# Kernel optimization log

Measured on AMD Instinct MI355X. Metric: run time of the kernel, lower is better.

The kernel has to match this reference:

```python
import jax, jax.numpy as jnp
import numpy as np

B, DIM, H, W = 8, 384, 64, 64
HEADS = 8
D = DIM // HEADS          # 48
D2 = D // 2               # 24
DU = D // 3 * 2           # 32 (ratio=3)


def setup_inputs() -> dict:
    key = jax.random.key(0)
    ks = jax.random.split(key, 12)
    s = lambda k, shape, scale=0.05: jax.random.normal(k, shape, jnp.float32) * scale
    return {
        "x": jax.random.normal(ks[0], (B, DIM, H, W), jnp.float32),
        "temperature": jnp.ones((HEADS, 1, 1), jnp.float32),
        "w_qkv": s(ks[1], (3 * DIM, DIM)),          # 1x1 conv, no bias
        "w_dw": s(ks[2], (3 * DIM, 1, 3, 3)),       # depthwise 3x3, groups=3*dim
        "w_proj": s(ks[3], (DIM, HEADS)),           # project_out 1x1
        "w_attn_r": s(ks[4], (1, D)),
        "w_v_r": s(ks[5], (D2, D)),
        "w_up1": s(ks[6], (DU, D2)),
        "b_up1": jnp.zeros((DU,), jnp.float32),
        "ln_w": jnp.ones((DU, HEADS, 1), jnp.float32),
        "ln_b": jnp.zeros((DU, HEADS, 1), jnp.float32),
        "w_up2": s(ks[7], (D, DU)),
        "b_up2": jnp.zeros((D,), jnp.float32),
        "w_attn_l": s(ks[8], (D2, D)),
        "w_v_l": s(ks[9], (D2, D)),
    }


def _qkv_attn(x, temperature, w_qkv, w_dw):
    # shared: qkv 1x1 conv -> depthwise 3x3 -> split, normalize, elementwise attn+softmax
    b, c, h, w = x.shape
    qkv = jnp.einsum('bchw,oc->bohw', x, w_qkv)
    qkv = jax.lax.conv_general_dilated(
        qkv, w_dw, (1, 1), 'SAME', feature_group_count=3 * c,
        dimension_numbers=('NCHW', 'OIHW', 'NCHW'))
    q, k, v = jnp.split(qkv, 3, axis=1)
    rs = lambda t: t.reshape(b, HEADS, D, h * w)  # b (head d) h w -> b head d (hw)
    q, k, v = rs(q), rs(k), rs(v)
    qn = q / jnp.maximum(jnp.linalg.norm(q, axis=-1, keepdims=True), 1e-12)
    kn = k / jnp.maximum(jnp.linalg.norm(k, axis=-1, keepdims=True), 1e-12)
    attn = jax.nn.softmax(qn * kn * temperature, axis=-1)  # [b, head, d, s]
    return attn, v


def _forward(x, temperature, w_qkv, w_dw, w_proj, w_attn_r, w_v_r,
             w_up1, b_up1, ln_w, ln_b, w_up2, b_up2, w_attn_l, w_v_l):
    b, c, h, w = x.shape
    attn, v = _qkv_attn(x, temperature, w_qkv, w_dw)

    # ---- spatial_pool (channel gating) ----
    input_x = jnp.einsum('bhds,od->bhos', v, w_v_r)                 # conv_v_right: [b,head,d2,s]
    cm = jax.nn.softmax(jnp.einsum('bhds,d->bhs', attn, w_attn_r[0]), axis=-1)  # conv_attn_right + softmax
    ctx = jnp.einsum('bhs,bhjs->bhj', cm, input_x)                  # [b,head,d2]
    ctx = ctx.transpose(0, 2, 1)[..., None]                         # [b, d2, head, 1]
    u = jnp.einsum('bchl,oc->bohl', ctx, w_up1) + b_up1[None, :, None, None]  # [b, DU, head, 1]
    mu = u.mean(axis=(1, 2, 3), keepdims=True)
    var = u.var(axis=(1, 2, 3), keepdims=True)
    u = (u - mu) / jnp.sqrt(var + 1e-5) * ln_w[None] + ln_b[None]   # LayerNorm([DU, 8, 1])
    u = jax.nn.relu(u)
    u = jnp.einsum('bchl,oc->bohl', u, w_up2) + b_up2[None, :, None, None]    # [b, D, head, 1]
    mask_ch = jax.nn.sigmoid(u).reshape(b, c, 1, 1)                 # view(b, head*D, 1, 1)
    out_channel = x * mask_ch

    # ---- channel_pool (spatial gating) ----
    g = jnp.einsum('bhds,od->bhos', attn, w_attn_l)                 # conv_attn_left: [b,head,d2,s]
    avg = jax.nn.softmax(g.mean(axis=-1), axis=-1)                  # avg-pool over s, softmax over d2
    theta = jnp.einsum('bhds,od->bhos', v, w_v_l)                   # conv_v_left: [b,head,d2,s]
    ctx2 = jnp.einsum('bhd,bhds->bhs', avg, theta)                  # matmul: [b,head,s]
    mask_sp = jax.nn.sigmoid(ctx2).reshape(b, HEADS, h, w)
    mask_sp = jnp.einsum('bchw,oc->bohw', mask_sp, w_proj)          # project_out
    out_spatial = x * mask_sp

    return out_spatial + out_channel


def reference(x, temperature, w_qkv, w_dw, w_proj, w_attn_r, w_v_r,
              w_up1, b_up1, ln_w, ln_b, w_up2, b_up2, w_attn_l, w_v_l):
    return _forward(x, temperature, w_qkv, w_dw, w_proj, w_attn_r, w_v_r,
                    w_up1, b_up1, ln_w, ln_b, w_up2, b_up2, w_attn_l, w_v_l)
```

## Files before the change

kernel.cpp:

```cpp
#include <hip/hip_runtime.h>
#include <math.h>


#define S4096 4096
#define C384  384
#define OC    1152

typedef unsigned short bfraw;
typedef unsigned int   u32;
typedef __attribute__((ext_vector_type(8))) short bf16x8;
typedef __attribute__((ext_vector_type(4))) float f32x4;

typedef __attribute__((address_space(3))) unsigned int lds_u32;
typedef const __attribute__((address_space(1))) unsigned int glb_u32;
__device__ __forceinline__ void gll16(const void* g, void* l) {
    __builtin_amdgcn_global_load_lds((glb_u32*)g, (lds_u32*)l, 16, 0, 0);
}

__device__ __forceinline__ bfraw f2bf(float f) {
    union { float f; u32 u; } c; c.f = f;
    u32 r = c.u + 0x7FFFu + ((c.u >> 16) & 1u);
    return (bfraw)(r >> 16);
}
__device__ __forceinline__ float bf2f(bfraw u) {
    union { u32 u; float f; } c; c.u = ((u32)u) << 16;
    return c.f;
}
__device__ __forceinline__ void unpack8(uint4 v, float* f) {
    f[0] = bf2f((bfraw)(v.x & 0xffff)); f[1] = bf2f((bfraw)(v.x >> 16));
    f[2] = bf2f((bfraw)(v.y & 0xffff)); f[3] = bf2f((bfraw)(v.y >> 16));
    f[4] = bf2f((bfraw)(v.z & 0xffff)); f[5] = bf2f((bfraw)(v.z >> 16));
    f[6] = bf2f((bfraw)(v.w & 0xffff)); f[7] = bf2f((bfraw)(v.w >> 16));
}
__device__ __forceinline__ uint4 pack8(const float* f) {
    union { bfraw us[8]; uint4 q; } p;
    #pragma unroll
    for (int i = 0; i < 8; i++) p.us[i] = f2bf(f[i]);
    return p.q;
}

__device__ __forceinline__ float blk_red(float v, float* s4, bool ismax) {
    #pragma unroll
    for (int off = 32; off; off >>= 1) {
        float o = __shfl_down(v, off, 64);
        v = ismax ? fmaxf(v, o) : (v + o);
    }
    __syncthreads();
    if ((threadIdx.x & 63) == 0) s4[threadIdx.x >> 6] = v;
    __syncthreads();
    return ismax ? fmaxf(fmaxf(s4[0], s4[1]), fmaxf(s4[2], s4[3]))
                 : ((s4[0] + s4[1]) + (s4[2] + s4[3]));
}

__global__ __launch_bounds__(256) void kA_prep(
    const float* __restrict__ w_qkv, bfraw* __restrict__ wF,
    const float* __restrict__ w_attn_l, const float* __restrict__ w_v_l,
    float* __restrict__ weff) {
    if (blockIdx.x == 216) {
        __shared__ float avg[24];
        const int tid = threadIdx.x;
        if (tid < 24) {
            float a = 0.f;
            for (int d = 0; d < 48; d++) a += w_attn_l[tid * 48 + d];
            avg[tid] = a * (1.f / 4096.f);
        }
        __syncthreads();
        if (tid == 0) {
            float M = -3.402823466e+38f;
            for (int o = 0; o < 24; o++) M = fmaxf(M, avg[o]);
            float S = 0.f;
            for (int o = 0; o < 24; o++) { avg[o] = __expf(avg[o] - M); S += avg[o]; }
            float inv = 1.f / S;
            for (int o = 0; o < 24; o++) avg[o] *= inv;
        }
        __syncthreads();
        if (tid < 48) {
            float a = 0.f;
            for (int o = 0; o < 24; o++) a += avg[o] * w_v_l[o * 48 + tid];
            weff[tid] = a;
        }
        return;
    }
    const int id = blockIdx.x * 256 + threadIdx.x;
    const int ob = id / 768, rem = id % 768;
    const int c = rem / 48, kb = rem % 48;
    const float* src = w_qkv + (size_t)(ob * 16 + c) * C384 + kb * 8;
    float f[8];
    *(float4*)f       = *(const float4*)src;
    *(float4*)(f + 4) = *(const float4*)(src + 4);
    *(uint4*)&wF[((size_t)(ob * 48 + kb) * 16 + c) * 8] = pack8(f);
}

__global__ __launch_bounds__(256) void kB_tr(
    const float* __restrict__ x, bfraw* __restrict__ xF, int b0) {
    const int cb = blockIdx.x, sb = blockIdx.y, bl = blockIdx.z;
    const int c0 = cb * 16, s0 = sb * 256;
    const int tid = threadIdx.x;
    __shared__ alignas(16) bfraw lt[16][264];
    {
        const int r = tid >> 4, seg = tid & 15;
        const float* src = x + ((size_t)(b0 + bl) * C384 + c0 + r) * S4096 + s0 + seg * 16;
        float f[16];
        #pragma unroll
        for (int i = 0; i < 4; i++) *(float4*)(f + i * 4) = *(const float4*)(src + i * 4);
        *(uint4*)&lt[r][seg * 16]     = pack8(f);
        *(uint4*)&lt[r][seg * 16 + 8] = pack8(f + 8);
    }
    __syncthreads();
    const int sbl = tid >> 4, c = tid & 15;
    bfraw* xFb = xF + (size_t)bl * S4096 * C384;
    #pragma unroll
    for (int kbl = 0; kbl < 2; kbl++) {
        union { bfraw us[8]; uint4 q; } p;
        #pragma unroll
        for (int j = 0; j < 8; j++) p.us[j] = lt[kbl * 8 + j][sbl * 16 + c];
        const size_t idx = (((size_t)((s0 >> 4) + sbl) * 48) + (c0 >> 3) + kbl) * 128 + c * 8;
        *(uint4*)&xFb[idx] = p.q;
    }
}

__global__ __launch_bounds__(256) void k1_gemm(
    const bfraw* __restrict__ wF, const bfraw* __restrict__ xF,
    bfraw* __restrict__ pre, int b0) {
    __shared__ alignas(16) bfraw smem[24576];
    const int tid = threadIdx.x;
    const int wave = tid >> 6, lane = tid & 63;
    const int sT = blockIdx.x, oT = blockIdx.y, bl = blockIdx.z;
    const bfraw* xFb = xF + (size_t)bl * S4096 * C384;

    const int c0_ = tid, c1_ = tid + 256;
    const int rb0 = c0_ >> 6, oc0 = (c0_ >> 4) & 3, rw0 = c0_ & 15;
    const int rb1 = c1_ >> 6, oc1 = (c1_ >> 4) & 3, rw1 = c1_ & 15;

    f32x4 acc[4][4];
    #pragma unroll
    for (int m = 0; m < 4; m++)
        #pragma unroll
        for (int n = 0; n < 4; n++) acc[m][n] = (f32x4){0, 0, 0, 0};

    const int wr = (wave >> 1) * 4;
    const int wc = (wave & 1) * 4;

    auto stage = [&](bfraw* dst, int kb0) {
        gll16(wF  + ((size_t)((oT * 8 + rb0) * 48 + kb0 + oc0) * 16 + rw0) * 8,
              dst + (size_t)c0_ * 8);
        gll16(wF  + ((size_t)((oT * 8 + rb1) * 48 + kb0 + oc1) * 16 + rw1) * 8,
              dst + (size_t)c1_ * 8);
        gll16(xFb + ((size_t)((sT * 8 + rb0) * 48 + kb0 + oc0) * 16 + rw0) * 8,
              dst + 4096 + (size_t)c0_ * 8);
        gll16(xFb + ((size_t)((sT * 8 + rb1) * 48 + kb0 + oc1) * 16 + rw1) * 8,
              dst + 4096 + (size_t)c1_ * 8);
    };

    stage(smem,        0);
    stage(smem + 8192, 4);

    #pragma unroll 3
    for (int ks = 0; ks < 12; ks++) {
        if (ks < 11) asm volatile("s_waitcnt vmcnt(4)" ::: "memory");
        else         asm volatile("s_waitcnt vmcnt(0)" ::: "memory");
        __builtin_amdgcn_s_barrier();
        const bfraw* cb = smem + (ks % 3) * 8192;
        bf16x8 af[4], bq[4];
        #pragma unroll
        for (int m = 0; m < 4; m++)
            af[m] = *(const bf16x8*)&cb[((wr + m) * 64 + lane) * 8];
        #pragma unroll
        for (int n = 0; n < 4; n++)
            bq[n] = *(const bf16x8*)&cb[4096 + ((wc + n) * 64 + lane) * 8];
        if (ks < 10) stage(smem + ((ks + 2) % 3) * 8192, (ks + 2) * 4);
        __builtin_amdgcn_s_setprio(1);
        #pragma unroll
        for (int m = 0; m < 4; m++)
            #pragma unroll
            for (int n = 0; n < 4; n++)
                acc[m][n] = __builtin_amdgcn_mfma_f32_16x16x32_bf16(af[m], bq[n], acc[m][n], 0, 0, 0);
        __builtin_amdgcn_s_setprio(0);
    }
    __syncthreads();

    const int er0 = (wave >> 1) * 64 + (lane >> 4) * 4;
    const int ec0 = (wave & 1) * 64 + (lane & 15);
    #pragma unroll
    for (int m = 0; m < 4; m++)
        #pragma unroll
        for (int n = 0; n < 4; n++)
            #pragma unroll
            for (int r = 0; r < 4; r++)
                smem[(er0 + m * 16 + r) * 136 + ec0 + n * 16] = f2bf(acc[m][n][r]);
    __syncthreads();
    const int row = tid >> 1, hh = tid & 1;
    bfraw* op = pre + (size_t)bl * OC * S4096
              + (size_t)(oT * 128 + row) * S4096 + sT * 128 + hh * 8;
    const bfraw* es = &smem[row * 136 + hh * 8];
    #pragma unroll
    for (int j = 0; j < 8; j++)
        *(uint4*)(op + j * 16) = *(const uint4*)(es + j * 16);
}

__device__ __forceinline__ void stencil8(const bfraw* plane, const float* w9,
                                         int ypad, int k7, int x0, float* acc) {
    #pragma unroll
    for (int j = 0; j < 8; j++) acc[j] = 0.f;
    #pragma unroll
    for (int dy = 0; dy < 3; dy++) {
        uint4 rv = *(const uint4*)&plane[(ypad + dy) * 64 + x0];
        float r[8]; unpack8(rv, r);
        float lft = __shfl_up(r[7], 1);
        float rgt = __shfl_down(r[0], 1);
        if (k7 == 0) lft = 0.f;
        if (k7 == 7) rgt = 0.f;
        const float w0 = w9[dy*3], w1 = w9[dy*3+1], w2 = w9[dy*3+2];
        acc[0] += w0*lft + w1*r[0] + w2*r[1];
        #pragma unroll
        for (int j = 1; j < 7; j++) acc[j] += w0*r[j-1] + w1*r[j] + w2*r[j+1];
        acc[7] += w0*r[6] + w1*r[7] + w2*rgt;
    }
}

__global__ __launch_bounds__(256) void k2f(
    const bfraw* __restrict__ pre, const float* __restrict__ w_dw,
    const float* __restrict__ temperature,
    bfraw* __restrict__ av, int b0) {
    const int idx = blockIdx.x;
    const int bl  = blockIdx.y;
    const int h   = idx / 48;
    const int tid = threadIdx.x;
    __shared__ alignas(16) bfraw pl[3][66 * 64];
    __shared__ float s4[4];

    const size_t pbase = (size_t)bl * OC * S4096;
    #pragma unroll
    for (int p = 0; p < 3; p++) {
        const bfraw* src = pre + pbase + (size_t)(idx + p * C384) * S4096;
        uint4 a = *(const uint4*)&src[tid * 16];
        uint4 b = *(const uint4*)&src[tid * 16 + 8];
        int y = tid >> 2, xq = (tid & 3) * 16;
        *(uint4*)&pl[p][(y + 1) * 64 + xq]     = a;
        *(uint4*)&pl[p][(y + 1) * 64 + xq + 8] = b;
    }
    if (tid < 64) {
        #pragma unroll
        for (int p = 0; p < 3; p++) { pl[p][tid] = 0; pl[p][65 * 64 + tid] = 0; }
    }
    float wq[9], wk[9], wv[9];
    #pragma unroll
    for (int i = 0; i < 9; i++) {
        wq[i] = w_dw[idx * 9 + i];
        wk[i] = w_dw[(idx + C384) * 9 + i];
        wv[i] = w_dw[(idx + 768) * 9 + i];
    }
    __syncthreads();

    const int sid0 = tid,        y0 = sid0 >> 3, k70 = sid0 & 7, x00 = k70 * 8;
    const int sid1 = tid + 256,  y1 = sid1 >> 3, k71 = sid1 & 7, x01 = k71 * 8;
    float qo[16], ko[16], vo[16];
    stencil8(pl[0], wq, y0, k70, x00, qo);
    stencil8(pl[0], wq, y1, k71, x01, qo + 8);
    stencil8(pl[1], wk, y0, k70, x00, ko);
    stencil8(pl[1], wk, y1, k71, x01, ko + 8);
    stencil8(pl[2], wv, y0, k70, x00, vo);
    stencil8(pl[2], wv, y1, k71, x01, vo + 8);

    float sq = 0.f, sk = 0.f;
    #pragma unroll
    for (int i = 0; i < 16; i++) { sq += qo[i] * qo[i]; sk += ko[i] * ko[i]; }
    float Sq = blk_red(sq, s4, false);
    float Sk = blk_red(sk, s4, false);
    float scale = temperature[h] /
        (fmaxf(sqrtf(Sq), 1e-12f) * fmaxf(sqrtf(Sk), 1e-12f));
    float lm = -3.402823466e+38f;
    #pragma unroll
    for (int i = 0; i < 16; i++) { qo[i] = qo[i] * ko[i] * scale; lm = fmaxf(lm, qo[i]); }
    float M = blk_red(lm, s4, true);
    float ls = 0.f;
    #pragma unroll
    for (int i = 0; i < 16; i++) { qo[i] = __expf(qo[i] - M); ls += qo[i]; }
    float Z = blk_red(ls, s4, false);
    float invZ = 1.f / Z;
    #pragma unroll
    for (int i = 0; i < 16; i++) qo[i] *= invZ;

    bfraw* adst = av + ((size_t)bl * 768 + idx) * S4096;
    bfraw* vdst = av + ((size_t)bl * 768 + 384 + idx) * S4096;
    *(uint4*)&adst[y0 * 64 + x00] = pack8(qo);
    *(uint4*)&adst[y1 * 64 + x01] = pack8(qo + 8);
    *(uint4*)&vdst[y0 * 64 + x00] = pack8(vo);
    *(uint4*)&vdst[y1 * 64 + x01] = pack8(vo + 8);
}

__global__ __launch_bounds__(256) void k4a(
    const bfraw* __restrict__ av, const float* __restrict__ w_attn_r,
    const float* __restrict__ weff,
    float* __restrict__ cmraw, float* __restrict__ c2raw, int b0) {
    const int h = blockIdx.x, bl = blockIdx.y, st = blockIdx.z;
    const int b = b0 + bl;
    const int tid = threadIdx.x;
    __shared__ float swr[48], swf[48];
    if (tid < 48) { swr[tid] = w_attn_r[tid]; swf[tid] = weff[tid]; }
    __syncthreads();
    const int s_off = st * 1024 + tid * 4;
    const bfraw* abase = av + ((size_t)bl * 768 + h * 48) * S4096 + s_off;
    const bfraw* vbase = abase + (size_t)384 * S4096;
    float cmr[4] = {0,0,0,0}, c2[4] = {0,0,0,0};
    for (int d = 0; d < 48; d++) {
        uint2 ua = *(const uint2*)(abase + (size_t)d * S4096);
        uint2 uv = *(const uint2*)(vbase + (size_t)d * S4096);
        const float wr = swr[d], wf = swf[d];
        cmr[0] += bf2f((bfraw)(ua.x & 0xffff)) * wr;
        cmr[1] += bf2f((bfraw)(ua.x >> 16))    * wr;
        cmr[2] += bf2f((bfraw)(ua.y & 0xffff)) * wr;
        cmr[3] += bf2f((bfraw)(ua.y >> 16))    * wr;
        c2[0]  += bf2f((bfraw)(uv.x & 0xffff)) * wf;
        c2[1]  += bf2f((bfraw)(uv.x >> 16))    * wf;
        c2[2]  += bf2f((bfraw)(uv.y & 0xffff)) * wf;
        c2[3]  += bf2f((bfraw)(uv.y >> 16))    * wf;
    }
    const size_t o = ((size_t)(b * 8 + h)) * S4096 + s_off;
    float4 a4 = {cmr[0], cmr[1], cmr[2], cmr[3]};
    float4 b4 = {c2[0], c2[1], c2[2], c2[3]};
    *(float4*)(cmraw + o) = a4;
    *(float4*)(c2raw + o) = b4;
}

__global__ __launch_bounds__(256) void k4b(
    const float* __restrict__ cmraw, const float* __restrict__ c2raw,
    bfraw* __restrict__ cmb, float* __restrict__ msp, int b0) {
    const int h = blockIdx.x, bl = blockIdx.y, b = b0 + bl;
    const int tid = threadIdx.x;
    __shared__ float s4[4];
    const size_t base = ((size_t)(b * 8 + h)) * S4096 + tid * 16;
    float v[16];
    #pragma unroll
    for (int i = 0; i < 4; i++) *(float4*)(v + i * 4) = *(const float4*)(cmraw + base + i * 4);
    float lm = -3.402823466e+38f;
    #pragma unroll
    for (int i = 0; i < 16; i++) lm = fmaxf(lm, v[i]);
    float M = blk_red(lm, s4, true);
    float ls = 0.f;
    #pragma unroll
    for (int i = 0; i < 16; i++) { v[i] = __expf(v[i] - M); ls += v[i]; }
    float Z = blk_red(ls, s4, false);
    float inv = 1.f / Z;
    #pragma unroll
    for (int i = 0; i < 16; i++) v[i] *= inv;
    *(uint4*)(cmb + base)     = pack8(v);
    *(uint4*)(cmb + base + 8) = pack8(v + 8);
    #pragma unroll
    for (int i = 0; i < 4; i++) {
        float4 c = *(const float4*)(c2raw + base + i * 4);
        float4 m;
        m.x = 1.f / (1.f + __expf(-c.x)); m.y = 1.f / (1.f + __expf(-c.y));
        m.z = 1.f / (1.f + __expf(-c.z)); m.w = 1.f / (1.f + __expf(-c.w));
        *(float4*)(msp + base + i * 4) = m;
    }
}

__global__ __launch_bounds__(256) void k5_vc(
    const bfraw* __restrict__ av, const bfraw* __restrict__ cmb,
    float* __restrict__ vc, int b0) {
    const int idx = blockIdx.x;
    const int bl = blockIdx.y, b = b0 + bl;
    const int h = idx / 48;
    const int tid = threadIdx.x;
    const bfraw* vr = av + ((size_t)bl * 768 + 384 + idx) * S4096 + tid * 16;
    const bfraw* cr = cmb + ((size_t)(b * 8 + h)) * S4096 + tid * 16;
    float vv[16], cc[16];
    { uint4 a = *(const uint4*)vr, c = *(const uint4*)(vr + 8); unpack8(a, vv); unpack8(c, vv + 8); }
    { uint4 a = *(const uint4*)cr, c = *(const uint4*)(cr + 8); unpack8(a, cc); unpack8(c, cc + 8); }
    float a = 0.f;
    #pragma unroll
    for (int i = 0; i < 16; i++) a += vv[i] * cc[i];
    __shared__ float s4[4];
    float S = blk_red(a, s4, false);
    if (tid == 0) vc[b * C384 + idx] = S;
}

__global__ __launch_bounds__(256) void k6_gate(
    const float* __restrict__ vc, const float* __restrict__ w_v_r,
    const float* __restrict__ w_up1, const float* __restrict__ b_up1,
    const float* __restrict__ ln_w, const float* __restrict__ ln_b,
    const float* __restrict__ w_up2, const float* __restrict__ b_up2,
    float* __restrict__ mch, int b0) {
    const int b = b0 + blockIdx.x;
    const int tid = threadIdx.x;
    __shared__ float s_vc[384], s_ctx[192], s_u[256], s4[4];
    for (int i = tid; i < 384; i += 256) s_vc[i] = vc[b * C384 + i];
    __syncthreads();
    if (tid < 192) {
        int hh = tid / 24, o = tid % 24;
        float a = 0.f;
        for (int d = 0; d < 48; d++) a += w_v_r[o * 48 + d] * s_vc[hh * 48 + d];
        s_ctx[hh * 24 + o] = a;
    }
    __syncthreads();
    float uval;
    {
        int o = tid >> 3, hh = tid & 7;
        float a = b_up1[o];
        for (int c = 0; c < 24; c++) a += w_up1[o * 24 + c] * s_ctx[hh * 24 + c];
        uval = a;
    }
    float mu  = blk_red(uval, s4, false) * (1.f / 256.f);
    float dv  = uval - mu;
    float var = blk_red(dv * dv, s4, false) * (1.f / 256.f);
    float un  = dv * rsqrtf(var + 1e-5f) * ln_w[tid] + ln_b[tid];
    s_u[tid] = fmaxf(un, 0.f);
    __syncthreads();
    for (int t = tid; t < 384; t += 256) {
        int o2 = t >> 3, hh = t & 7;
        float a = b_up2[o2];
        for (int o = 0; o < 32; o++) a += w_up2[o2 * 32 + o] * s_u[o * 8 + hh];
        mch[b * C384 + t] = 1.f / (1.f + __expf(-a));
    }
}

__global__ __launch_bounds__(256) void k7_out(
    const float* __restrict__ x, const float* __restrict__ w_proj,
    const float* __restrict__ mch, const float* __restrict__ msp,
    float* __restrict__ out, int b0) {
    const int st = blockIdx.x, cg = blockIdx.y, bl = blockIdx.z;
    const int b = b0 + bl;
    const int tid = threadIdx.x;
    const int s0 = st * 256, c0 = cg * 48;
    __shared__ float s_msp[8][256];
    __shared__ float s_mch[48];
    __shared__ float s_wp[48][8];
    for (int i = tid; i < 2048; i += 256) {
        int hh = i >> 8, ss = i & 255;
        s_msp[hh][ss] = msp[((size_t)(b * 8 + hh)) * S4096 + s0 + ss];
    }
    if (tid < 48) s_mch[tid] = mch[b * C384 + c0 + tid];
    for (int i = tid; i < 384; i += 256)
        s_wp[i >> 3][i & 7] = w_proj[(size_t)(c0 + (i >> 3)) * 8 + (i & 7)];
    __syncthreads();

    const int cl = tid >> 6;
    const int s4i = (tid & 63) * 4;
    float4 m[8];
    #pragma unroll
    for (int hh = 0; hh < 8; hh++) m[hh] = *(const float4*)&s_msp[hh][s4i];

    #pragma unroll 4
    for (int j = 0; j < 12; j++) {
        const int cloc = j * 4 + cl;
        const int c = c0 + cloc;
        const float base = s_mch[cloc];
        float4 a = {base, base, base, base};
        #pragma unroll
        for (int hh = 0; hh < 8; hh++) {
            const float wp = s_wp[cloc][hh];
            a.x += wp * m[hh].x; a.y += wp * m[hh].y;
            a.z += wp * m[hh].z; a.w += wp * m[hh].w;
        }
        const size_t o = ((size_t)b * C384 + c) * S4096 + s0 + s4i;
        float4 xv = *(const float4*)(x + o);
        a.x *= xv.x; a.y *= xv.y; a.z *= xv.z; a.w *= xv.w;
        *(float4*)(out + o) = a;
    }
}

extern "C" void kernel_launch(void* const* d_in, const int* in_sizes, int n_in,
                              void* d_out, int out_size, void* d_ws, size_t ws_size,
                              hipStream_t stream) {
    const float* x        = (const float*)d_in[0];
    const float* temp     = (const float*)d_in[1];
    const float* w_qkv    = (const float*)d_in[2];
    const float* w_dw     = (const float*)d_in[3];
    const float* w_proj   = (const float*)d_in[4];
    const float* w_attn_r = (const float*)d_in[5];
    const float* w_v_r    = (const float*)d_in[6];
    const float* w_up1    = (const float*)d_in[7];
    const float* b_up1    = (const float*)d_in[8];
    const float* ln_w     = (const float*)d_in[9];
    const float* ln_b     = (const float*)d_in[10];
    const float* w_up2    = (const float*)d_in[11];
    const float* b_up2    = (const float*)d_in[12];
    const float* w_attn_l = (const float*)d_in[13];
    const float* w_v_l    = (const float*)d_in[14];
    float* out = (float*)d_out;
    char* ws = (char*)d_ws;

    size_t off = 0;
    auto alloc = [&](size_t bytes) {
        size_t o = off; off = (off + bytes + 255) & ~(size_t)255; return o;
    };
    float* cmraw = (float*)(ws + alloc((size_t)64 * S4096 * 4));
    float* c2raw = (float*)(ws + alloc((size_t)64 * S4096 * 4));
    bfraw* cmb   = (bfraw*)(ws + alloc((size_t)64 * S4096 * 2));
    float* msp   = (float*)(ws + alloc((size_t)64 * S4096 * 4));
    float* vc    = (float*)(ws + alloc(3072 * 4));
    float* mch   = (float*)(ws + alloc(3072 * 4));
    float* weff  = (float*)(ws + alloc(256));
    bfraw* wF    = (bfraw*)(ws + alloc((size_t)55296 * 16));
    const size_t big_xF  = (size_t)S4096 * C384 * 2;
    const size_t big_pre = (size_t)OC * S4096 * 2;
    const size_t big_av  = (size_t)768 * S4096 * 2;
    int nb = (ws_size >= off + 8 * (big_xF + big_pre + big_av)) ? 8 : 1;
    bfraw* xF  = (bfraw*)(ws + alloc((size_t)nb * big_xF));
    bfraw* pre = (bfraw*)(ws + alloc((size_t)nb * big_pre));
    bfraw* av  = (bfraw*)(ws + alloc((size_t)nb * big_av));

    kA_prep<<<217, 256, 0, stream>>>(w_qkv, wF, w_attn_l, w_v_l, weff);
    for (int b0 = 0; b0 < 8; b0 += nb) {
        kB_tr<<<dim3(24, 16, nb), 256, 0, stream>>>(x, xF, b0);
        k1_gemm<<<dim3(32, 9, nb), 256, 0, stream>>>(wF, xF, pre, b0);
        k2f<<<dim3(384, nb), 256, 0, stream>>>(pre, w_dw, temp, av, b0);
        k4a<<<dim3(8, nb, 4), 256, 0, stream>>>(av, w_attn_r, weff, cmraw, c2raw, b0);
        k4b<<<dim3(8, nb), 256, 0, stream>>>(cmraw, c2raw, cmb, msp, b0);
        k5_vc<<<dim3(384, nb), 256, 0, stream>>>(av, cmb, vc, b0);
        k6_gate<<<dim3(nb), 256, 0, stream>>>(vc, w_v_r, w_up1, b_up1,
                                              ln_w, ln_b, w_up2, b_up2, mch, b0);
        k7_out<<<dim3(16, 8, nb), 256, 0, stream>>>(x, w_proj, mch, msp, out, b0);
    }
}
```

Before: 126.8 us.

## Make GEMM blocks persistent over four spatial tiles and store intermediates in bf16

```diff
diff --git a/kernel.cpp b/kernel.cpp
--- a/kernel.cpp
+++ b/kernel.cpp
@@ -125,13 +125,27 @@
     __shared__ alignas(16) bfraw smem[24576];
     const int tid = threadIdx.x;
     const int wave = tid >> 6, lane = tid & 63;
-    const int sT = blockIdx.x, oT = blockIdx.y, bl = blockIdx.z;
+    const int sG = blockIdx.x, oT = blockIdx.y, bl = blockIdx.z;
     const bfraw* xFb = xF + (size_t)bl * S4096 * C384;
 
     const int c0_ = tid, c1_ = tid + 256;
     const int rb0 = c0_ >> 6, oc0 = (c0_ >> 4) & 3, rw0 = c0_ & 15;
     const int rb1 = c1_ >> 6, oc1 = (c1_ >> 4) & 3, rw1 = c1_ & 15;
 
+    const bfraw* pA0 = wF + ((size_t)((oT * 8 + rb0) * 48 + oc0) * 16 + rw0) * 8;
+    const bfraw* pA1 = wF + ((size_t)((oT * 8 + rb1) * 48 + oc1) * 16 + rw1) * 8;
+    const bfraw* pB0 = xFb + ((size_t)((sG * 32 + rb0) * 48 + oc0) * 16 + rw0) * 8;
+    const bfraw* pB1 = xFb + ((size_t)((sG * 32 + rb1) * 48 + oc1) * 16 + rw1) * 8;
+
+    auto stage = [&](bfraw* dst, int ks, int st) {
+        const int ko = ks * 512;
+        const int so = st * 49152 + ko;
+        gll16(pA0 + ko, dst + (size_t)c0_ * 8);
+        gll16(pA1 + ko, dst + (size_t)c1_ * 8);
+        gll16(pB0 + so, dst + 4096 + (size_t)c0_ * 8);
+        gll16(pB1 + so, dst + 4096 + (size_t)c1_ * 8);
+    };
+
     f32x4 acc[4][4];
     #pragma unroll
     for (int m = 0; m < 4; m++)
@@ -140,27 +154,19 @@
 
     const int wr = (wave >> 1) * 4;
     const int wc = (wave & 1) * 4;
-
-    auto stage = [&](bfraw* dst, int kb0) {
-        gll16(wF  + ((size_t)((oT * 8 + rb0) * 48 + kb0 + oc0) * 16 + rw0) * 8,
-              dst + (size_t)c0_ * 8);
-        gll16(wF  + ((size_t)((oT * 8 + rb1) * 48 + kb0 + oc1) * 16 + rw1) * 8,
-              dst + (size_t)c1_ * 8);
-        gll16(xFb + ((size_t)((sT * 8 + rb0) * 48 + kb0 + oc0) * 16 + rw0) * 8,
-              dst + 4096 + (size_t)c0_ * 8);
-        gll16(xFb + ((size_t)((sT * 8 + rb1) * 48 + kb0 + oc1) * 16 + rw1) * 8,
-              dst + 4096 + (size_t)c1_ * 8);
-    };
-
-    stage(smem,        0);
-    stage(smem + 8192, 4);
-
-    #pragma unroll 3
-    for (int ks = 0; ks < 12; ks++) {
-        if (ks < 11) asm volatile("s_waitcnt vmcnt(4)" ::: "memory");
-        else         asm volatile("s_waitcnt vmcnt(0)" ::: "memory");
+    const int orow0 = oT * 128 + (wave >> 1) * 64 + (lane >> 4) * 4;
+    bfraw* op = pre + (size_t)bl * OC * S4096;
+
+    stage(smem,        0, 0);
+    stage(smem + 8192, 1, 0);
+    int ks_p = 2, st_p = 0, bp = 2;
+    int ks_c = 0, st_c = 0, bi = 0;
+
+    for (int i = 0; i < 48; ++i) {
+        if (i < 47) asm volatile("s_waitcnt vmcnt(4)" ::: "memory");
+        else        asm volatile("s_waitcnt vmcnt(0)" ::: "memory");
         __builtin_amdgcn_s_barrier();
-        const bfraw* cb = smem + (ks % 3) * 8192;
+        const bfraw* cb = smem + bi * 8192;
         bf16x8 af[4], bq[4];
         #pragma unroll
         for (int m = 0; m < 4; m++)
@@ -168,7 +174,11 @@
         #pragma unroll
         for (int n = 0; n < 4; n++)
             bq[n] = *(const bf16x8*)&cb[4096 + ((wc + n) * 64 + lane) * 8];
-        if (ks < 10) stage(smem + ((ks + 2) % 3) * 8192, (ks + 2) * 4);
+        if (i < 46) {
+            stage(smem + bp * 8192, ks_p, st_p);
+            if (++ks_p == 12) { ks_p = 0; ++st_p; }
+            bp = (bp == 2) ? 0 : bp + 1;
+        }
         __builtin_amdgcn_s_setprio(1);
         #pragma unroll
         for (int m = 0; m < 4; m++)
@@ -176,26 +186,23 @@
             for (int n = 0; n < 4; n++)
                 acc[m][n] = __builtin_amdgcn_mfma_f32_16x16x32_bf16(af[m], bq[n], acc[m][n], 0, 0, 0);
         __builtin_amdgcn_s_setprio(0);
-    }
-    __syncthreads();
-
-    const int er0 = (wave >> 1) * 64 + (lane >> 4) * 4;
-    const int ec0 = (wave & 1) * 64 + (lane & 15);
-    #pragma unroll
-    for (int m = 0; m < 4; m++)
-        #pragma unroll
-        for (int n = 0; n < 4; n++)
+        if (++ks_c == 12) {
+            const int scol0 = (sG * 4 + st_c) * 128 + (wave & 1) * 64 + (lane & 15);
             #pragma unroll
-            for (int r = 0; r < 4; r++)
-                smem[(er0 + m * 16 + r) * 136 + ec0 + n * 16] = f2bf(acc[m][n][r]);
-    __syncthreads();
-    const int row = tid >> 1, hh = tid & 1;
-    bfraw* op = pre + (size_t)bl * OC * S4096
-              + (size_t)(oT * 128 + row) * S4096 + sT * 128 + hh * 8;
-    const bfraw* es = &smem[row * 136 + hh * 8];
-    #pragma unroll
-    for (int j = 0; j < 8; j++)
-        *(uint4*)(op + j * 16) = *(const uint4*)(es + j * 16);
+            for (int m = 0; m < 4; m++)
+                #pragma unroll
+                for (int n = 0; n < 4; n++)
+                    #pragma unroll
+                    for (int r = 0; r < 4; r++)
+                        op[(size_t)(orow0 + m * 16 + r) * S4096 + scol0 + n * 16] = f2bf(acc[m][n][r]);
+            #pragma unroll
+            for (int m = 0; m < 4; m++)
+                #pragma unroll
+                for (int n = 0; n < 4; n++) acc[m][n] = (f32x4){0, 0, 0, 0};
+            ks_c = 0; ++st_c;
+        }
+        bi = (bi == 2) ? 0 : bi + 1;
+    }
 }
 
 __device__ __forceinline__ void stencil8(const bfraw* plane, const float* w9,
@@ -292,7 +299,7 @@
 __global__ __launch_bounds__(256) void k4a(
     const bfraw* __restrict__ av, const float* __restrict__ w_attn_r,
     const float* __restrict__ weff,
-    float* __restrict__ cmraw, float* __restrict__ c2raw, int b0) {
+    bfraw* __restrict__ cmraw, bfraw* __restrict__ c2raw, int b0) {
     const int h = blockIdx.x, bl = blockIdx.y, st = blockIdx.z;
     const int b = b0 + bl;
     const int tid = threadIdx.x;
@@ -317,22 +324,23 @@
         c2[3]  += bf2f((bfraw)(uv.y >> 16))    * wf;
     }
     const size_t o = ((size_t)(b * 8 + h)) * S4096 + s_off;
-    float4 a4 = {cmr[0], cmr[1], cmr[2], cmr[3]};
-    float4 b4 = {c2[0], c2[1], c2[2], c2[3]};
-    *(float4*)(cmraw + o) = a4;
-    *(float4*)(c2raw + o) = b4;
+    union { bfraw us[4]; uint2 q; } pa, pb;
+    #pragma unroll
+    for (int j = 0; j < 4; j++) { pa.us[j] = f2bf(cmr[j]); pb.us[j] = f2bf(c2[j]); }
+    *(uint2*)(cmraw + o) = pa.q;
+    *(uint2*)(c2raw + o) = pb.q;
 }
 
 __global__ __launch_bounds__(256) void k4b(
-    const float* __restrict__ cmraw, const float* __restrict__ c2raw,
-    bfraw* __restrict__ cmb, float* __restrict__ msp, int b0) {
+    const bfraw* __restrict__ cmraw, const bfraw* __restrict__ c2raw,
+    bfraw* __restrict__ cmb, bfraw* __restrict__ msp, int b0) {
     const int h = blockIdx.x, bl = blockIdx.y, b = b0 + bl;
     const int tid = threadIdx.x;
     __shared__ float s4[4];
     const size_t base = ((size_t)(b * 8 + h)) * S4096 + tid * 16;
     float v[16];
-    #pragma unroll
-    for (int i = 0; i < 4; i++) *(float4*)(v + i * 4) = *(const float4*)(cmraw + base + i * 4);
+    { uint4 a = *(const uint4*)(cmraw + base), c = *(const uint4*)(cmraw + base + 8);
+      unpack8(a, v); unpack8(c, v + 8); }
     float lm = -3.402823466e+38f;
     #pragma unroll
     for (int i = 0; i < 16; i++) lm = fmaxf(lm, v[i]);
@@ -346,14 +354,13 @@
     for (int i = 0; i < 16; i++) v[i] *= inv;
     *(uint4*)(cmb + base)     = pack8(v);
     *(uint4*)(cmb + base + 8) = pack8(v + 8);
-    #pragma unroll
-    for (int i = 0; i < 4; i++) {
-        float4 c = *(const float4*)(c2raw + base + i * 4);
-        float4 m;
-        m.x = 1.f / (1.f + __expf(-c.x)); m.y = 1.f / (1.f + __expf(-c.y));
-        m.z = 1.f / (1.f + __expf(-c.z)); m.w = 1.f / (1.f + __expf(-c.w));
-        *(float4*)(msp + base + i * 4) = m;
-    }
+    float sg[16];
+    { uint4 a = *(const uint4*)(c2raw + base), c = *(const uint4*)(c2raw + base + 8);
+      unpack8(a, sg); unpack8(c, sg + 8); }
+    #pragma unroll
+    for (int i = 0; i < 16; i++) sg[i] = 1.f / (1.f + __expf(-sg[i]));
+    *(uint4*)(msp + base)     = pack8(sg);
+    *(uint4*)(msp + base + 8) = pack8(sg + 8);
 }
 
 __global__ __launch_bounds__(256) void k5_vc(
@@ -417,7 +424,7 @@
 
 __global__ __launch_bounds__(256) void k7_out(
     const float* __restrict__ x, const float* __restrict__ w_proj,
-    const float* __restrict__ mch, const float* __restrict__ msp,
+    const float* __restrict__ mch, const bfraw* __restrict__ msp,
     float* __restrict__ out, int b0) {
     const int st = blockIdx.x, cg = blockIdx.y, bl = blockIdx.z;
     const int b = b0 + bl;
@@ -428,7 +435,7 @@
     __shared__ float s_wp[48][8];
     for (int i = tid; i < 2048; i += 256) {
         int hh = i >> 8, ss = i & 255;
-        s_msp[hh][ss] = msp[((size_t)(b * 8 + hh)) * S4096 + s0 + ss];
+        s_msp[hh][ss] = bf2f(msp[((size_t)(b * 8 + hh)) * S4096 + s0 + ss]);
     }
     if (tid < 48) s_mch[tid] = mch[b * C384 + c0 + tid];
     for (int i = tid; i < 384; i += 256)
@@ -485,10 +492,10 @@
     auto alloc = [&](size_t bytes) {
         size_t o = off; off = (off + bytes + 255) & ~(size_t)255; return o;
     };
-    float* cmraw = (float*)(ws + alloc((size_t)64 * S4096 * 4));
-    float* c2raw = (float*)(ws + alloc((size_t)64 * S4096 * 4));
+    bfraw* cmraw = (bfraw*)(ws + alloc((size_t)64 * S4096 * 2));
+    bfraw* c2raw = (bfraw*)(ws + alloc((size_t)64 * S4096 * 2));
     bfraw* cmb   = (bfraw*)(ws + alloc((size_t)64 * S4096 * 2));
-    float* msp   = (float*)(ws + alloc((size_t)64 * S4096 * 4));
+    bfraw* msp   = (bfraw*)(ws + alloc((size_t)64 * S4096 * 2));
     float* vc    = (float*)(ws + alloc(3072 * 4));
     float* mch   = (float*)(ws + alloc(3072 * 4));
     float* weff  = (float*)(ws + alloc(256));
@@ -504,7 +511,7 @@
     kA_prep<<<217, 256, 0, stream>>>(w_qkv, wF, w_attn_l, w_v_l, weff);
     for (int b0 = 0; b0 < 8; b0 += nb) {
         kB_tr<<<dim3(24, 16, nb), 256, 0, stream>>>(x, xF, b0);
-        k1_gemm<<<dim3(32, 9, nb), 256, 0, stream>>>(wF, xF, pre, b0);
+        k1_gemm<<<dim3(8, 9, nb), 256, 0, stream>>>(wF, xF, pre, b0);
         k2f<<<dim3(384, nb), 256, 0, stream>>>(pre, w_dw, temp, av, b0);
         k4a<<<dim3(8, nb, 4), 256, 0, stream>>>(av, w_attn_r, weff, cmraw, c2raw, b0);
         k4b<<<dim3(8, nb), 256, 0, stream>>>(cmraw, c2raw, cmb, msp, b0);
```

Result: slower. 136.9 us (+7.9%).
